# Performance work log

Hardware: AMD Instinct MI355X
Metric: run time of the kernel (lower is better)

The kernel has to match this reference:

```python
import jax, jax.numpy as jnp
import numpy as np

T, B, IN_DIM, H = 512, 256, 512, 256  # H == hidden_dim == n_qubits

def setup_inputs() -> dict:
    key = jax.random.key(0)
    ks = jax.random.split(key, 13)
    inputs = jax.random.normal(ks[0], (T, B, IN_DIM), dtype=jnp.float32)
    d = IN_DIM + H
    s = 1.0 / np.sqrt(d)
    def lin(k):
        k1, k2 = jax.random.split(k)
        return (jax.random.uniform(k1, (H, d), jnp.float32, -s, s),
                jax.random.uniform(k2, (H,), jnp.float32, -s, s))
    Wf, bf = lin(ks[1]); Wi, bi = lin(ks[2]); Wg, bg = lin(ks[3]); Wo, bo = lin(ks[4])
    thf = jax.random.uniform(ks[5], (H,), jnp.float32)
    thi = jax.random.uniform(ks[6], (H,), jnp.float32)
    thg = jax.random.uniform(ks[7], (H,), jnp.float32)
    tho = jax.random.uniform(ks[8], (H,), jnp.float32)
    return dict(inputs=inputs, Wf=Wf, bf=bf, thf=thf, Wi=Wi, bi=bi, thi=thi,
                Wg=Wg, bg=bg, thg=thg, Wo=Wo, bo=bo, tho=tho)

def _qgate(combined, W, b, th):
    # Analytic form of the RY+RY+CNOT-ladder circuit with PauliZ expvals:
    # <Z_k> = prod_{i<=k} cos(z_i + theta_i), z = Linear(combined)
    z = combined @ W.T + b  # [B, H]
    return jnp.cumprod(jnp.cos(z + th), axis=-1)

def reference(inputs, Wf, bf, thf, Wi, bi, thi, Wg, bg, thg, Wo, bo, tho):
    batch = inputs.shape[1]
    hx0 = jnp.zeros((batch, H), inputs.dtype)
    cx0 = jnp.zeros((batch, H), inputs.dtype)

    def step(carry, x):
        hx, cx = carry
        comb = jnp.concatenate([x, hx], axis=1)  # [B, IN_DIM+H]
        f = jax.nn.sigmoid(_qgate(comb, Wf, bf, thf))
        i = jax.nn.sigmoid(_qgate(comb, Wi, bi, thi))
        g = jnp.tanh(_qgate(comb, Wg, bg, thg))
        o = jax.nn.sigmoid(_qgate(comb, Wo, bo, tho))
        cx = f * cx + i * g
        hx = o * jnp.tanh(cx)
        return (hx, cx), hx

    (hx, cx), stacked = jax.lax.scan(step, (hx0, cx0), inputs)
    return stacked, hx, cx
```

## Files before the change

kernel.cpp:

```cpp
#include <hip/hip_runtime.h>
#include <hip/hip_bf16.h>
#include <stdint.h>

#define T_STEPS 512
#define BATCH   256
#define HID     256

#define NRWG   64
#define NWWG   192
#define NWG    256
#define RING   4
#define CHUNK  8
#define NCHUNK 64
#define TPC    64
#define SLOT_F (CHUNK*256*1024)

using short8 = __attribute__((ext_vector_type(8))) short;
using f32x4  = __attribute__((ext_vector_type(4))) float;

#define VMCNT0() asm volatile("s_waitcnt vmcnt(0)" ::: "memory")

__device__ inline unsigned short f2bf(float f) {
  unsigned u = __float_as_uint(f);
  unsigned r = (u + 0x7fffu + ((u >> 16) & 1u)) >> 16;
  return (unsigned short)r;
}
__device__ inline float sigm(float x)   { return __builtin_amdgcn_rcpf(1.0f + __expf(-x)); }
__device__ inline float tanh_f(float x) { return 2.0f * __builtin_amdgcn_rcpf(1.0f + __expf(-2.0f * x)) - 1.0f; }

__device__ inline int ld_rlx(const int* p) {
  return __hip_atomic_load(p, __ATOMIC_RELAXED, __HIP_MEMORY_SCOPE_AGENT);
}
__device__ inline void add_rlx(int* p, int v) {
  __hip_atomic_fetch_add(p, v, __ATOMIC_RELAXED, __HIP_MEMORY_SCOPE_AGENT);
}
__device__ inline float ldg_coh(const float* p) {
  return __hip_atomic_load(p, __ATOMIC_RELAXED, __HIP_MEMORY_SCOPE_AGENT);
}
__device__ inline void stg_coh(float* p, float v) {
  __hip_atomic_store(p, v, __ATOMIC_RELAXED, __HIP_MEMORY_SCOPE_AGENT);
}
__device__ inline void st16_coh(f32x4* p, f32x4 v) {
  asm volatile("global_store_dwordx4 %0, %1, off sc0 sc1" :: "v"(p), "v"(v) : "memory");
}

__device__ inline int hswz(int byte) { return byte ^ (((byte >> 8) & 3) << 4); }

struct RecSm {
  unsigned short hL[4096];
  float z[8][520];
};
struct GemSm { unsigned short aL[4096]; unsigned short bL[8192]; };

__global__ __launch_bounds__(256) void prep_kernel(
    const float* __restrict__ Wf, const float* __restrict__ Wi,
    const float* __restrict__ Wg, const float* __restrict__ Wo,
    const float* __restrict__ bf_, const float* __restrict__ bi_,
    const float* __restrict__ bg_, const float* __restrict__ bo_,
    const float* __restrict__ thf, const float* __restrict__ thi,
    const float* __restrict__ thg, const float* __restrict__ tho,
    unsigned short* __restrict__ Wfull, float* __restrict__ cvec,
    int* __restrict__ flags, float* __restrict__ pk)
{
  int j = blockIdx.x;
  int g = j >> 8, col = j & 255;
  const float* W  = (g==0)?Wf:(g==1)?Wi:(g==2)?Wg:Wo;
  const float* bb = (g==0)?bf_:(g==1)?bi_:(g==2)?bg_:bo_;
  const float* th = (g==0)?thf:(g==1)?thi:(g==2)?thg:tho;
  const float* wrow = W + (size_t)col * 768;
  for (int k = threadIdx.x; k < 768; k += blockDim.x)
    Wfull[(size_t)j * 768 + k] = f2bf(wrow[k]);
  if (threadIdx.x == 0) cvec[j] = bb[col] + th[col];
  if (j == 0) for (int i = threadIdx.x; i < 512; i += 256) flags[i] = 0;
  float* pz = pk + (size_t)j * 768;
  for (int i = threadIdx.x; i < 768; i += 256) pz[i] = 0.0f;
}

__global__ __launch_bounds__(512, 2) void persist_kernel(
    const float* __restrict__ X,
    const unsigned short* __restrict__ Wfull,
    const float* __restrict__ cvec,
    float* __restrict__ ring,
    f32x4* __restrict__ pk,
    int* __restrict__ done,
    int* __restrict__ consumed,
    float* __restrict__ out)
{
  __shared__ union { RecSm rec; GemSm gem; } sm;

  int bid = blockIdx.x, tid = threadIdx.x;
  int lane = tid & 63, wv = tid >> 6;
  int l15 = lane & 15, lk = lane >> 4;

  if (bid < NRWG) {
    int bg = bid >> 1, half = bid & 1;

    for (int i = tid; i < 4096; i += 512) sm.rec.hL[i] = 0;

    short8 af[4][8];
#pragma unroll
    for (int st = 0; st < 4; ++st)
#pragma unroll
      for (int kk = 0; kk < 8; ++kk)
        af[st][kk] = *(const short8*)(Wfull +
            (size_t)(half*512 + wv*64 + st*16 + l15)*768 + 512 + kk*32 + lk*8);

    float creg[4] = {0.f, 0.f, 0.f, 0.f};
    float zx[8];
    __syncthreads();

    for (int t = 0; t < T_STEPS; ++t) {
      int cIdx = t >> 3;
      if ((t & 7) == 0) {
        if (tid == 0) { while (ld_rlx(&done[cIdx]) < TPC) __builtin_amdgcn_s_sleep(1); }
        __syncthreads();
        const float* zp = ring + (size_t)(cIdx & (RING-1))*SLOT_F
                        + ((size_t)(bg*8 + wv))*1024 + half*512 + lane;
#pragma unroll
        for (int s = 0; s < 8; ++s) zx[s] = ldg_coh(zp + s*64);
      }

      short8 bfr[8];
#pragma unroll
      for (int kk = 0; kk < 8; ++kk)
        bfr[kk] = *(const short8*)((const char*)sm.rec.hL + hswz(kk*1024 + lane*16));
      f32x4 acc[4];
#pragma unroll
      for (int st = 0; st < 4; ++st) acc[st] = (f32x4){0.f,0.f,0.f,0.f};
#pragma unroll
      for (int kk = 0; kk < 8; ++kk)
#pragma unroll
        for (int st = 0; st < 4; ++st)
          acc[st] = __builtin_amdgcn_mfma_f32_16x16x32_bf16(af[st][kk], bfr[kk], acc[st], 0, 0, 0);
      if (l15 < 8) {
#pragma unroll
        for (int st = 0; st < 4; ++st)
          *(f32x4*)&sm.rec.z[l15][wv*64 + st*16 + lk*4] = acc[st];
      }
      __syncthreads();

      float v[8];
#pragma unroll
      for (int s = 0; s < 8; ++s)
        v[s] = __cosf(sm.rec.z[wv][s*64 + lane] + zx[s]);
#pragma unroll
      for (int off = 1; off < 64; off <<= 1) {
        float u[8];
#pragma unroll
        for (int s = 0; s < 8; ++s) u[s] = __shfl_up(v[s], (unsigned)off, 64);
        if (lane >= off) {
#pragma unroll
          for (int s = 0; s < 8; ++s) v[s] *= u[s];
        }
      }
      float tA0 = __shfl(v[0], 63, 64), tA1 = __shfl(v[1], 63, 64), tA2 = __shfl(v[2], 63, 64);
      float tB0 = __shfl(v[4], 63, 64), tB1 = __shfl(v[5], 63, 64), tB2 = __shfl(v[6], 63, 64);
      float pA2 = tA0*tA1, pA3 = pA2*tA2;
      float pB2 = tB0*tB1, pB3 = pB2*tB2;
      float aA[4] = {v[0], v[1]*tA0, v[2]*pA2, v[3]*pA3};
      float aB[4] = {v[4], v[5]*tB0, v[6]*pB2, v[7]*pB3};
      if (half == 0) {
#pragma unroll
        for (int s = 0; s < 4; ++s) { aA[s] = sigm(aA[s]); aB[s] = sigm(aB[s]); }
      } else {
#pragma unroll
        for (int s = 0; s < 4; ++s) { aA[s] = tanh_f(aA[s]); aB[s] = sigm(aB[s]); }
      }

      int par = t & 1, T1 = t + 1;
      float seqf = __int_as_float(T1);
      size_t idx = ((((size_t)par*32 + bg)*2 + half)*8 + wv)*64 + lane;
      f32x4* myp = pk + idx*3;
      f32x4 P0 = {aA[0], aA[1], aA[2], seqf};
      f32x4 P1 = {aA[3], aB[0], aB[1], seqf};
      f32x4 P2 = {aB[2], aB[3], 0.f,  seqf};
      st16_coh(myp,     P0);
      st16_coh(myp + 1, P1);
      st16_coh(myp + 2, P2);

      if (((t+1) & 7) != 0 && t+1 < T_STEPS) {
        const float* zp = ring + (size_t)(cIdx & (RING-1))*SLOT_F
                        + ((size_t)(((t+1) & 7)*256) + bg*8 + wv)*1024 + half*512 + lane;
#pragma unroll
        for (int s = 0; s < 8; ++s) zx[s] = ldg_coh(zp + s*64);
      }

      size_t pidx = ((((size_t)par*32 + bg)*2 + (half^1))*8 + wv)*64 + lane;
      const f32x4* pp = pk + pidx*3;
      f32x4 q0, q1, q2;
      do {
        asm volatile(
          "global_load_dwordx4 %0, %3, off sc0 sc1\n\t"
          "global_load_dwordx4 %1, %4, off sc0 sc1\n\t"
          "global_load_dwordx4 %2, %5, off sc0 sc1\n\t"
          "s_waitcnt vmcnt(0)"
          : "=&v"(q0), "=&v"(q1), "=&v"(q2)
          : "v"(pp), "v"(pp + 1), "v"(pp + 2)
          : "memory");
      } while (__float_as_int(q0[3]) < T1 || __float_as_int(q1[3]) < T1 ||
               __float_as_int(q2[3]) < T1);
      float p0 = q0[0], p1 = q0[1], p2 = q0[2], p3 = q1[0];
      float p4 = q1[1], p5 = q1[2], p6 = q2[0], p7 = q2[1];

      float fv[4], iv[4], gv[4], ov[4];
      if (half == 0) {
#pragma unroll
        for (int s = 0; s < 4; ++s) { fv[s] = aA[s]; iv[s] = aB[s]; }
        gv[0]=p0; gv[1]=p1; gv[2]=p2; gv[3]=p3;
        ov[0]=p4; ov[1]=p5; ov[2]=p6; ov[3]=p7;
      } else {
#pragma unroll
        for (int s = 0; s < 4; ++s) { gv[s] = aA[s]; ov[s] = aB[s]; }
        fv[0]=p0; fv[1]=p1; fv[2]=p2; fv[3]=p3;
        iv[0]=p4; iv[1]=p5; iv[2]=p6; iv[3]=p7;
      }

      int brow = bg*8 + wv;
#pragma unroll
      for (int s = 0; s < 4; ++s) {
        float cn = fv[s]*creg[s] + iv[s]*gv[s];
        creg[s] = cn;
        float h = ov[s]*tanh_f(cn);
        int k = s*64 + lane;
        int byte = (k >> 5)*1024 + ((((k >> 3) & 3)*16 + wv)*16) + (k & 7)*2;
        *(unsigned short*)((char*)sm.rec.hL + hswz(byte)) = f2bf(h);
        if (half == 0) {
          out[(size_t)t*(BATCH*HID) + (size_t)brow*256 + k] = h;
          if (t == T_STEPS-1) {
            out[(size_t)T_STEPS*(BATCH*HID) + (size_t)brow*256 + k] = h;
            out[(size_t)T_STEPS*(BATCH*HID) + BATCH*HID + (size_t)brow*256 + k] = cn;
          }
        }
      }
      if ((t & 7) == 7 && tid == 0) add_rlx(consumed, 1);
      __syncthreads();
    }
  } else {
    int w0 = bid - NRWG;
    int wr = wv >> 2, wc = wv & 3;
    int rA = tid >> 2, kA = (tid & 3) * 8;
    int rB = tid >> 1, kB = (tid & 1) * 16;

    for (int gt = w0; gt < NCHUNK * TPC; gt += NWWG) {
      int c  = gt >> 6;
      int tl = gt & 63;
      int tm = tl >> 2, tn = tl & 3;

      int need = NRWG * (c - RING + 1);
      if (need > 0) {
        if (tid == 0) { while (ld_rlx(consumed) < need) __builtin_amdgcn_s_sleep(8); }
        __syncthreads();
      }

      const float* Xb = X + ((size_t)c*(CHUNK*256) + (size_t)tm*128) * 512;
      float* slotp = ring + (size_t)(c & (RING-1)) * SLOT_F;

      f32x4 acc[4][4];
#pragma unroll
      for (int mi = 0; mi < 4; ++mi)
#pragma unroll
        for (int ni = 0; ni < 4; ++ni) acc[mi][ni] = (f32x4){0.f,0.f,0.f,0.f};

      int slotA = (rA >> 4)*1024 + ((tid & 3)*16 + (rA & 15))*16;
      int baseB = (rB >> 4)*1024;
      int kO = kB >> 3;
      int slotB0 = baseB + ((kO    )*16 + (rB & 15))*16;
      int slotB1 = baseB + ((kO + 1)*16 + (rB & 15))*16;

      for (int kb = 0; kb < 512; kb += 32) {
        const float* ap = Xb + (size_t)rA*512 + kb + kA;
        f32x4 v0 = *(const f32x4*)ap;
        f32x4 v1 = *(const f32x4*)(ap + 4);
        unsigned short t8[8];
        t8[0]=f2bf(v0[0]); t8[1]=f2bf(v0[1]); t8[2]=f2bf(v0[2]); t8[3]=f2bf(v0[3]);
        t8[4]=f2bf(v1[0]); t8[5]=f2bf(v1[1]); t8[6]=f2bf(v1[2]); t8[7]=f2bf(v1[3]);
        *(short8*)((char*)sm.gem.aL + slotA) = *(short8*)t8;
        const unsigned short* bp = Wfull + (size_t)(tn*256 + rB)*768 + kb + kB;
        *(short8*)((char*)sm.gem.bL + slotB0) = *(const short8*)bp;
        *(short8*)((char*)sm.gem.bL + slotB1) = *(const short8*)(bp + 8);
        __syncthreads();

        short8 afr[4], bfr4[4];
#pragma unroll
        for (int mi = 0; mi < 4; ++mi)
          afr[mi]  = *(const short8*)((const char*)sm.gem.aL + (wr*4 + mi)*1024 + lane*16);
#pragma unroll
        for (int ni = 0; ni < 4; ++ni)
          bfr4[ni] = *(const short8*)((const char*)sm.gem.bL + (wc*4 + ni)*1024 + lane*16);
#pragma unroll
        for (int mi = 0; mi < 4; ++mi)
#pragma unroll
          for (int ni = 0; ni < 4; ++ni)
            acc[mi][ni] = __builtin_amdgcn_mfma_f32_16x16x32_bf16(afr[mi], bfr4[ni], acc[mi][ni], 0, 0, 0);
        __syncthreads();
      }

#pragma unroll
      for (int mi = 0; mi < 4; ++mi) {
#pragma unroll
        for (int ni = 0; ni < 4; ++ni) {
          int col = tn*256 + wc*64 + ni*16 + l15;
          float cv = cvec[col];
#pragma unroll
          for (int reg = 0; reg < 4; ++reg) {
            int row = tm*128 + wr*64 + mi*16 + lk*4 + reg;
            stg_coh(&slotp[(size_t)row*1024 + col], acc[mi][ni][reg] + cv);
          }
        }
      }
      VMCNT0();
      __syncthreads();
      if (tid == 0) add_rlx(&done[c], 1);
    }
  }
}

extern "C" void kernel_launch(void* const* d_in, const int* in_sizes, int n_in,
                              void* d_out, int out_size, void* d_ws, size_t ws_size,
                              hipStream_t stream) {
  const float* x   = (const float*)d_in[0];
  const float* Wf  = (const float*)d_in[1];
  const float* bf_ = (const float*)d_in[2];
  const float* thf = (const float*)d_in[3];
  const float* Wi  = (const float*)d_in[4];
  const float* bi_ = (const float*)d_in[5];
  const float* thi = (const float*)d_in[6];
  const float* Wg  = (const float*)d_in[7];
  const float* bg_ = (const float*)d_in[8];
  const float* thg = (const float*)d_in[9];
  const float* Wo  = (const float*)d_in[10];
  const float* bo_ = (const float*)d_in[11];
  const float* tho = (const float*)d_in[12];
  float* out = (float*)d_out;

  char* ws = (char*)d_ws;
  unsigned short* Wfull = (unsigned short*)ws;
  float* cvec  = (float*)(ws + 1572864);
  int*   flags = (int*)(ws + 1576960);
  f32x4* pk    = (f32x4*)(ws + 2097152);
  float* ring  = (float*)(ws + 8388608);

  prep_kernel<<<1024, 256, 0, stream>>>(Wf, Wi, Wg, Wo, bf_, bi_, bg_, bo_,
                                        thf, thi, thg, tho, Wfull, cvec, flags,
                                        (float*)pk);
  persist_kernel<<<NWG, 512, 0, stream>>>(x, Wfull, cvec, ring, pk,
                                          flags, flags + 128, out);
}
```

Measured before the change: 2.712 ms.

## Give each recurrent workgroup all four gates for 16 batch rows

Recurrent workgroups drop from 64 to 16, and each now computes all 4 gates × 256 hidden units for 16 batch rows. This removes the cross-workgroup exchange of gate activations through global memory and its spin-wait. Recurrent weights can no longer stay in registers, so they are streamed from global/L2 every step with double-buffered loads. The x-projection ring is read per step instead of per chunk, and readiness of the next chunk is polled ahead of time. The 48 freed workgroups go to the input-projection GEMM, at the cost of more weight traffic on the serial critical path.

```diff
diff --git a/kernel.cpp b/kernel.cpp
--- a/kernel.cpp
+++ b/kernel.cpp
@@ -6,8 +6,8 @@
 #define BATCH   256
 #define HID     256
 
-#define NRWG   64
-#define NWWG   192
+#define NRC    16
+#define NWWG   240
 #define NWG    256
 #define RING   4
 #define CHUNK  8
@@ -16,6 +16,7 @@
 #define SLOT_F (CHUNK*256*1024)
 
 using short8 = __attribute__((ext_vector_type(8))) short;
+using us4    = __attribute__((ext_vector_type(4))) unsigned short;
 using f32x4  = __attribute__((ext_vector_type(4))) float;
 
 #define VMCNT0() asm volatile("s_waitcnt vmcnt(0)" ::: "memory")
@@ -40,15 +41,13 @@
 __device__ inline void stg_coh(float* p, float v) {
   __hip_atomic_store(p, v, __ATOMIC_RELAXED, __HIP_MEMORY_SCOPE_AGENT);
 }
-__device__ inline void st16_coh(f32x4* p, f32x4 v) {
-  asm volatile("global_store_dwordx4 %0, %1, off sc0 sc1" :: "v"(p), "v"(v) : "memory");
-}
 
 __device__ inline int hswz(int byte) { return byte ^ (((byte >> 8) & 3) << 4); }
 
 struct RecSm {
   unsigned short hL[4096];
-  float z[8][520];
+  float z[16][1028];
+  int rdy;
 };
 struct GemSm { unsigned short aL[4096]; unsigned short bL[8192]; };
 
@@ -60,7 +59,7 @@
     const float* __restrict__ thf, const float* __restrict__ thi,
     const float* __restrict__ thg, const float* __restrict__ tho,
     unsigned short* __restrict__ Wfull, float* __restrict__ cvec,
-    int* __restrict__ flags, float* __restrict__ pk)
+    int* __restrict__ flags)
 {
   int j = blockIdx.x;
   int g = j >> 8, col = j & 255;
@@ -72,8 +71,6 @@
     Wfull[(size_t)j * 768 + k] = f2bf(wrow[k]);
   if (threadIdx.x == 0) cvec[j] = bb[col] + th[col];
   if (j == 0) for (int i = threadIdx.x; i < 512; i += 256) flags[i] = 0;
-  float* pz = pk + (size_t)j * 768;
-  for (int i = threadIdx.x; i < 768; i += 256) pz[i] = 0.0f;
 }
 
 __global__ __launch_bounds__(512, 2) void persist_kernel(
@@ -81,7 +78,6 @@
     const unsigned short* __restrict__ Wfull,
     const float* __restrict__ cvec,
     float* __restrict__ ring,
-    f32x4* __restrict__ pk,
     int* __restrict__ done,
     int* __restrict__ consumed,
     float* __restrict__ out)
@@ -92,151 +88,148 @@
   int lane = tid & 63, wv = tid >> 6;
   int l15 = lane & 15, lk = lane >> 4;
 
-  if (bid < NRWG) {
-    int bg = bid >> 1, half = bid & 1;
+  if (bid < NRC) {
+    int bg = bid;
+    int cs = wv * 128;
+    int r0 = wv * 2;
 
     for (int i = tid; i < 4096; i += 512) sm.rec.hL[i] = 0;
-
-    short8 af[4][8];
-#pragma unroll
-    for (int st = 0; st < 4; ++st)
-#pragma unroll
-      for (int kk = 0; kk < 8; ++kk)
-        af[st][kk] = *(const short8*)(Wfull +
-            (size_t)(half*512 + wv*64 + st*16 + l15)*768 + 512 + kk*32 + lk*8);
-
-    float creg[4] = {0.f, 0.f, 0.f, 0.f};
-    float zx[8];
+    if (tid == 0) sm.rec.rdy = 0;
+
+    f32x4 cr[2] = {(f32x4){0.f,0.f,0.f,0.f}, (f32x4){0.f,0.f,0.f,0.f}};
     __syncthreads();
 
     for (int t = 0; t < T_STEPS; ++t) {
       int cIdx = t >> 3;
+
       if ((t & 7) == 0) {
-        if (tid == 0) { while (ld_rlx(&done[cIdx]) < TPC) __builtin_amdgcn_s_sleep(1); }
-        __syncthreads();
-        const float* zp = ring + (size_t)(cIdx & (RING-1))*SLOT_F
-                        + ((size_t)(bg*8 + wv))*1024 + half*512 + lane;
-#pragma unroll
-        for (int s = 0; s < 8; ++s) zx[s] = ldg_coh(zp + s*64);
-      }
-
-      short8 bfr[8];
+        if (sm.rec.rdy < TPC) {
+          if (tid == 0) { while (ld_rlx(&done[cIdx]) < TPC) __builtin_amdgcn_s_sleep(1); }
+          __syncthreads();
+        }
+      }
+
+      short8 aA[8], aB[8];
+#pragma unroll
+      for (int ct = 0; ct < 8; ++ct)
+        aA[ct] = *(const short8*)(Wfull + (size_t)(cs + ct*16 + l15)*768 + 512 + lk*8);
+
+      const float* slot = ring + (size_t)(cIdx & (RING-1))*SLOT_F
+                        + (size_t)(t & 7)*256*1024;
+      float zx[2][4][4];
+#pragma unroll
+      for (int r = 0; r < 2; ++r) {
+        const float* zp = slot + (size_t)(bg*16 + r0 + r)*1024 + 4*lane;
+#pragma unroll
+        for (int g = 0; g < 4; ++g)
+#pragma unroll
+          for (int j = 0; j < 4; ++j)
+            zx[r][g][j] = ldg_coh(zp + g*256 + j);
+      }
+
+      short8 hb[8];
 #pragma unroll
       for (int kk = 0; kk < 8; ++kk)
-        bfr[kk] = *(const short8*)((const char*)sm.rec.hL + hswz(kk*1024 + lane*16));
-      f32x4 acc[4];
-#pragma unroll
-      for (int st = 0; st < 4; ++st) acc[st] = (f32x4){0.f,0.f,0.f,0.f};
-#pragma unroll
-      for (int kk = 0; kk < 8; ++kk)
-#pragma unroll
-        for (int st = 0; st < 4; ++st)
-          acc[st] = __builtin_amdgcn_mfma_f32_16x16x32_bf16(af[st][kk], bfr[kk], acc[st], 0, 0, 0);
-      if (l15 < 8) {
-#pragma unroll
-        for (int st = 0; st < 4; ++st)
-          *(f32x4*)&sm.rec.z[l15][wv*64 + st*16 + lk*4] = acc[st];
-      }
+        hb[kk] = *(const short8*)((const char*)sm.rec.hL + hswz(kk*1024 + lane*16));
+
+      f32x4 acc[8];
+#pragma unroll
+      for (int ct = 0; ct < 8; ++ct) acc[ct] = (f32x4){0.f,0.f,0.f,0.f};
+#pragma unroll
+      for (int kk = 0; kk < 8; ++kk) {
+        short8* ac = (kk & 1) ? aB : aA;
+        short8* an = (kk & 1) ? aA : aB;
+        if (kk < 7) {
+#pragma unroll
+          for (int ct = 0; ct < 8; ++ct)
+            an[ct] = *(const short8*)(Wfull + (size_t)(cs + ct*16 + l15)*768 + 512 + (kk+1)*32 + lk*8);
+        }
+#pragma unroll
+        for (int ct = 0; ct < 8; ++ct)
+          acc[ct] = __builtin_amdgcn_mfma_f32_16x16x32_bf16(ac[ct], hb[kk], acc[ct], 0, 0, 0);
+      }
+#pragma unroll
+      for (int ct = 0; ct < 8; ++ct)
+        *(f32x4*)&sm.rec.z[l15][cs + ct*16 + lk*4] = acc[ct];
       __syncthreads();
 
-      float v[8];
-#pragma unroll
-      for (int s = 0; s < 8; ++s)
-        v[s] = __cosf(sm.rec.z[wv][s*64 + lane] + zx[s]);
+      float vv[2][4][4];
+#pragma unroll
+      for (int r = 0; r < 2; ++r)
+#pragma unroll
+        for (int g = 0; g < 4; ++g) {
+          f32x4 zz = *(const f32x4*)&sm.rec.z[r0 + r][g*256 + 4*lane];
+#pragma unroll
+          for (int j = 0; j < 4; ++j)
+            vv[r][g][j] = __cosf(zz[j] + zx[r][g][j]);
+        }
+      float S[8];
+#pragma unroll
+      for (int k = 0; k < 8; ++k) {
+        int r = k >> 2, g = k & 3;
+        S[k] = vv[r][g][0]*vv[r][g][1]*vv[r][g][2]*vv[r][g][3];
+      }
 #pragma unroll
       for (int off = 1; off < 64; off <<= 1) {
         float u[8];
 #pragma unroll
-        for (int s = 0; s < 8; ++s) u[s] = __shfl_up(v[s], (unsigned)off, 64);
+        for (int k = 0; k < 8; ++k) u[k] = __shfl_up(S[k], (unsigned)off, 64);
         if (lane >= off) {
 #pragma unroll
-          for (int s = 0; s < 8; ++s) v[s] *= u[s];
-        }
-      }
-      float tA0 = __shfl(v[0], 63, 64), tA1 = __shfl(v[1], 63, 64), tA2 = __shfl(v[2], 63, 64);
-      float tB0 = __shfl(v[4], 63, 64), tB1 = __shfl(v[5], 63, 64), tB2 = __shfl(v[6], 63, 64);
-      float pA2 = tA0*tA1, pA3 = pA2*tA2;
-      float pB2 = tB0*tB1, pB3 = pB2*tB2;
-      float aA[4] = {v[0], v[1]*tA0, v[2]*pA2, v[3]*pA3};
-      float aB[4] = {v[4], v[5]*tB0, v[6]*pB2, v[7]*pB3};
-      if (half == 0) {
-#pragma unroll
-        for (int s = 0; s < 4; ++s) { aA[s] = sigm(aA[s]); aB[s] = sigm(aB[s]); }
-      } else {
-#pragma unroll
-        for (int s = 0; s < 4; ++s) { aA[s] = tanh_f(aA[s]); aB[s] = sigm(aB[s]); }
-      }
-
-      int par = t & 1, T1 = t + 1;
-      float seqf = __int_as_float(T1);
-      size_t idx = ((((size_t)par*32 + bg)*2 + half)*8 + wv)*64 + lane;
-      f32x4* myp = pk + idx*3;
-      f32x4 P0 = {aA[0], aA[1], aA[2], seqf};
-      f32x4 P1 = {aA[3], aB[0], aB[1], seqf};
-      f32x4 P2 = {aB[2], aB[3], 0.f,  seqf};
-      st16_coh(myp,     P0);
-      st16_coh(myp + 1, P1);
-      st16_coh(myp + 2, P2);
-
-      if (((t+1) & 7) != 0 && t+1 < T_STEPS) {
-        const float* zp = ring + (size_t)(cIdx & (RING-1))*SLOT_F
-                        + ((size_t)(((t+1) & 7)*256) + bg*8 + wv)*1024 + half*512 + lane;
-#pragma unroll
-        for (int s = 0; s < 8; ++s) zx[s] = ldg_coh(zp + s*64);
-      }
-
-      size_t pidx = ((((size_t)par*32 + bg)*2 + (half^1))*8 + wv)*64 + lane;
-      const f32x4* pp = pk + pidx*3;
-      f32x4 q0, q1, q2;
-      do {
-        asm volatile(
-          "global_load_dwordx4 %0, %3, off sc0 sc1\n\t"
-          "global_load_dwordx4 %1, %4, off sc0 sc1\n\t"
-          "global_load_dwordx4 %2, %5, off sc0 sc1\n\t"
-          "s_waitcnt vmcnt(0)"
-          : "=&v"(q0), "=&v"(q1), "=&v"(q2)
-          : "v"(pp), "v"(pp + 1), "v"(pp + 2)
-          : "memory");
-      } while (__float_as_int(q0[3]) < T1 || __float_as_int(q1[3]) < T1 ||
-               __float_as_int(q2[3]) < T1);
-      float p0 = q0[0], p1 = q0[1], p2 = q0[2], p3 = q1[0];
-      float p4 = q1[1], p5 = q1[2], p6 = q2[0], p7 = q2[1];
-
-      float fv[4], iv[4], gv[4], ov[4];
-      if (half == 0) {
-#pragma unroll
-        for (int s = 0; s < 4; ++s) { fv[s] = aA[s]; iv[s] = aB[s]; }
-        gv[0]=p0; gv[1]=p1; gv[2]=p2; gv[3]=p3;
-        ov[0]=p4; ov[1]=p5; ov[2]=p6; ov[3]=p7;
-      } else {
-#pragma unroll
-        for (int s = 0; s < 4; ++s) { gv[s] = aA[s]; ov[s] = aB[s]; }
-        fv[0]=p0; fv[1]=p1; fv[2]=p2; fv[3]=p3;
-        iv[0]=p4; iv[1]=p5; iv[2]=p6; iv[3]=p7;
-      }
-
-      int brow = bg*8 + wv;
-#pragma unroll
-      for (int s = 0; s < 4; ++s) {
-        float cn = fv[s]*creg[s] + iv[s]*gv[s];
-        creg[s] = cn;
-        float h = ov[s]*tanh_f(cn);
-        int k = s*64 + lane;
-        int byte = (k >> 5)*1024 + ((((k >> 3) & 3)*16 + wv)*16) + (k & 7)*2;
-        *(unsigned short*)((char*)sm.rec.hL + hswz(byte)) = f2bf(h);
-        if (half == 0) {
-          out[(size_t)t*(BATCH*HID) + (size_t)brow*256 + k] = h;
-          if (t == T_STEPS-1) {
-            out[(size_t)T_STEPS*(BATCH*HID) + (size_t)brow*256 + k] = h;
-            out[(size_t)T_STEPS*(BATCH*HID) + BATCH*HID + (size_t)brow*256 + k] = cn;
-          }
-        }
-      }
+          for (int k = 0; k < 8; ++k) S[k] *= u[k];
+        }
+      }
+      float E[8];
+#pragma unroll
+      for (int k = 0; k < 8; ++k) {
+        float e = __shfl_up(S[k], 1u, 64);
+        E[k] = (lane == 0) ? 1.0f : e;
+      }
+
+      float av[2][4][4];
+#pragma unroll
+      for (int r = 0; r < 2; ++r)
+#pragma unroll
+        for (int g = 0; g < 4; ++g) {
+          int k = r*4 + g;
+          float o0 = E[k]*vv[r][g][0];
+          float o1 = o0  *vv[r][g][1];
+          float o2 = o1  *vv[r][g][2];
+          float o3 = o2  *vv[r][g][3];
+          if (g == 2) { av[r][g][0]=tanh_f(o0); av[r][g][1]=tanh_f(o1);
+                        av[r][g][2]=tanh_f(o2); av[r][g][3]=tanh_f(o3); }
+          else        { av[r][g][0]=sigm(o0);   av[r][g][1]=sigm(o1);
+                        av[r][g][2]=sigm(o2);   av[r][g][3]=sigm(o3); }
+        }
+
+#pragma unroll
+      for (int r = 0; r < 2; ++r) {
+        float hv[4];
+#pragma unroll
+        for (int j = 0; j < 4; ++j) {
+          float cn = av[r][0][j]*cr[r][j] + av[r][1][j]*av[r][2][j];
+          cr[r][j] = cn;
+          hv[j] = av[r][3][j]*tanh_f(cn);
+        }
+        int k = 4*lane;
+        int byte = (k >> 5)*1024 + ((k >> 3) & 3)*256 + (r0 + r)*16 + (k & 7)*2;
+        us4 hp = { f2bf(hv[0]), f2bf(hv[1]), f2bf(hv[2]), f2bf(hv[3]) };
+        *(us4*)((char*)sm.rec.hL + hswz(byte)) = hp;
+        int brow = bg*16 + r0 + r;
+        f32x4 ho = { hv[0], hv[1], hv[2], hv[3] };
+        *(f32x4*)&out[(size_t)t*(BATCH*HID) + (size_t)brow*256 + 4*lane] = ho;
+        if (t == T_STEPS-1) {
+          *(f32x4*)&out[(size_t)T_STEPS*(BATCH*HID) + (size_t)brow*256 + 4*lane] = ho;
+          *(f32x4*)&out[(size_t)T_STEPS*(BATCH*HID) + BATCH*HID + (size_t)brow*256 + 4*lane] = cr[r];
+        }
+      }
+
+      if (tid == 0) sm.rec.rdy = ld_rlx(&done[cIdx + 1]);
       if ((t & 7) == 7 && tid == 0) add_rlx(consumed, 1);
       __syncthreads();
     }
   } else {
-    int w0 = bid - NRWG;
+    int w0 = bid - NRC;
     int wr = wv >> 2, wc = wv & 3;
     int rA = tid >> 2, kA = (tid & 3) * 8;
     int rB = tid >> 1, kB = (tid & 1) * 16;
@@ -246,7 +239,7 @@
       int tl = gt & 63;
       int tm = tl >> 2, tn = tl & 3;
 
-      int need = NRWG * (c - RING + 1);
+      int need = NRC * (c - RING + 1);
       if (need > 0) {
         if (tid == 0) { while (ld_rlx(consumed) < need) __builtin_amdgcn_s_sleep(8); }
         __syncthreads();
@@ -337,12 +330,10 @@
   unsigned short* Wfull = (unsigned short*)ws;
   float* cvec  = (float*)(ws + 1572864);
   int*   flags = (int*)(ws + 1576960);
-  f32x4* pk    = (f32x4*)(ws + 2097152);
-  float* ring  = (float*)(ws + 8388608);
+  float* ring  = (float*)(ws + 4194304);
 
   prep_kernel<<<1024, 256, 0, stream>>>(Wf, Wi, Wg, Wo, bf_, bi_, bg_, bo_,
-                                        thf, thi, thg, tho, Wfull, cvec, flags,
-                                        (float*)pk);
-  persist_kernel<<<NWG, 512, 0, stream>>>(x, Wfull, cvec, ring, pk,
+                                        thf, thi, thg, tho, Wfull, cvec, flags);
+  persist_kernel<<<NWG, 512, 0, stream>>>(x, Wfull, cvec, ring,
                                           flags, flags + 128, out);
 }
```

After: 7.172 ms. 2.64x slower.
